# Kernel optimization log

Measured on AMD Instinct MI355X. Metric: run time of the kernel, lower is better.

The kernel has to match this reference:

```python
import jax, jax.numpy as jnp
import numpy as np

B = 16384    # batch of game states
HAND = 8     # max_hand_size
A = 30       # max_actions
C = 4        # max cards per action combo
E = 32       # card_embed_dim
HID = 128    # hidden_dim


def _encode_cards(cards, val_emb, suit_emb, type_emb):
    # cards: int array, 0 = padding, 53 = joker (treated as padding for value/suit)
    invalid = (cards == 0) | (cards == 53)
    values = jnp.where(invalid, 0, (cards - 1) % 13 + 1)
    suits = jnp.where(invalid, 0, (cards - 1) // 13 + 1)
    ce = jnp.concatenate([val_emb[values], suit_emb[suits]], axis=-1)  # [..., E]
    ct = jnp.where(values == 11, 1, jnp.where(values == 12, 2, jnp.where(values == 13, 3, 0)))
    te = type_emb[ct]  # [..., 8]
    pad = jnp.zeros(te.shape[:-1] + (E - te.shape[-1],), ce.dtype)
    return ce + jnp.concatenate([te, pad], axis=-1)


def _mha(q, kv, wq, bq, wk, bk, wv, bv, wo, bo, nh, kpm=None):
    b, sq, e = q.shape
    sk = kv.shape[1]
    hd = e // nh
    Q = (q @ wq + bq).reshape(b, sq, nh, hd)
    K = (kv @ wk + bk).reshape(b, sk, nh, hd)
    V = (kv @ wv + bv).reshape(b, sk, nh, hd)
    s = jnp.einsum('bqhd,bkhd->bhqk', Q, K) * (1.0 / np.sqrt(hd))
    if kpm is not None:  # kpm True = valid key
        s = s + jnp.where(kpm[:, None, None, :], 0.0, -1e9)
    a = jax.nn.softmax(s, axis=-1)
    o = jnp.einsum('bhqk,bkhd->bqhd', a, V).reshape(b, sq, e)
    return o @ wo + bo


def _combo_features(cards):
    # cards: [A, C] int, 0 = padding. Vectorized version of _compute_combo_features.
    mask = cards != 0
    combo_size = mask.sum(1).astype(jnp.float32)
    values = jnp.where(mask, (cards - 1) % 13 + 1, 0)
    has_valid = mask.any(1)
    fidx = jnp.argmax(mask, axis=1)
    fv = values[jnp.arange(cards.shape[0]), fidx]  # first valid value per action
    same = jnp.where(mask, values == fv[:, None], True).all(1).astype(jnp.float32)
    vf = values.astype(jnp.float32)
    attack = jnp.where(values == 1, 1.0,
             jnp.where(values == 11, 10.0,
             jnp.where(values == 12, 15.0,
             jnp.where(values == 13, 20.0, vf))))
    total = (attack * mask).sum(1)
    suits = jnp.where(mask, (cards - 1) // 13 + 1, 0)
    uniq = jnp.stack([(suits == s).any(1) for s in (1, 2, 3, 4)], 0).sum(0).astype(jnp.float32)
    ace = ((values == 1) & mask).any(1).astype(jnp.float32)
    valid = ((combo_size <= 4.0) & ((same > 0) | (ace > 0))).astype(jnp.float32)
    feats = jnp.stack([combo_size, same, total, uniq, ace, valid], axis=1)  # [A, 6]
    return jnp.where(has_valid[:, None], feats, 0.0), has_valid


def _forward(hand_cards, enemy_card, hand_size, game_state, discard_pile_cards,
             action_card_indices, num_valid_actions,
             val_emb, suit_emb, type_emb,
             ce_w1, ce_b1, ce_w2, ce_b2,
             ha_wq, ha_bq, ha_wk, ha_bk, ha_wv, ha_bv, ha_wo, ha_bo,
             he_wq, he_bq, he_wk, he_bk, he_wv, he_bv, he_wo, he_bo,
             se_w1, se_b1, se_w2, se_b2,
             atc_w1, atc_b1, atc_w2, atc_b2,
             as_w1, as_b1, as_w2, as_b2, as_w3, as_b3,
             cx_w1, cx_b1, cx_w2, cx_b2, cx_w3, cx_b3):
    relu = jax.nn.relu
    hand_emb = _encode_cards(hand_cards, val_emb, suit_emb, type_emb)            # [B, HAND, E]
    enemy_emb = _encode_cards(enemy_card[:, None], val_emb, suit_emb, type_emb)  # [B, 1, E]
    hand_mask = hand_cards != 0
    attended = _mha(hand_emb, hand_emb, ha_wq, ha_bq, ha_wk, ha_bk, ha_wv, ha_bv, ha_wo, ha_bo, 8, kpm=hand_mask)
    ctx_he = _mha(attended, enemy_emb, he_wq, he_bq, he_wk, he_bk, he_wv, he_bv, he_wo, he_bo, 4)
    lengths = jnp.maximum(hand_size.astype(jnp.float32), 1.0)[:, None]
    hand_ctx = ctx_he.sum(1) / lengths                                           # [B, E]

    # strategic features (batched per game state)
    hvals = jnp.where(hand_cards == 0, 0, (hand_cards - 1) % 13 + 1)
    hsz = hand_size.astype(jnp.float32)
    aces = (hvals == 1).sum(1).astype(jnp.float32)
    faces = ((hvals >= 11) & (hvals <= 13)).sum(1).astype(jnp.float32)
    low = ((hvals >= 2) & (hvals <= 6)).sum(1).astype(jnp.float32)
    hsuits = jnp.where(hand_cards == 0, 0, (hand_cards - 1) // 13 + 1)
    scnt = [(hsuits == s).sum(1).astype(jnp.float32) for s in (1, 2, 3, 4)]
    hvr = faces / (hsz + 1e-8)
    sdiv = jnp.stack([(hsuits == s).any(1) for s in (1, 2, 3, 4)], 0).sum(0).astype(jnp.float32) / 4.0
    strat = jnp.stack([hsz, aces, faces, low, scnt[0], scnt[1], scnt[2], scnt[3], hvr, sdiv], axis=1)
    strat_in = jnp.concatenate([game_state, strat], axis=1)                      # [B, 20]
    strat_ctx = relu(strat_in @ se_w1 + se_b1) @ se_w2 + se_b2                   # [B, 32]

    combined = jnp.concatenate([hand_ctx, enemy_emb[:, 0], strat_ctx, discard_pile_cards], axis=1)  # [B, 150]
    h = relu(combined @ cx_w1 + cx_b1)
    h = relu(h @ cx_w2 + cx_b2)
    ctx = h @ cx_w3 + cx_b3                                                      # [B, HID]
    type_probs = jax.nn.softmax(relu(ctx @ atc_w1 + atc_b1) @ atc_w2 + atc_b2, axis=-1)  # [B, 4]

    feats, has_valid = _combo_features(action_card_indices)                      # [A, 6], [A]
    emb = _encode_cards(action_card_indices, val_emb, suit_emb, type_emb)        # [A, C, E]
    m = (action_card_indices != 0).astype(emb.dtype)[..., None]
    cnt = jnp.maximum(m.sum(1), 1.0)
    act_emb = (emb * m).sum(1) / cnt                                             # masked mean over real cards
    act_emb = jnp.where(has_valid[:, None], act_emb, 0.0)
    combo_enc = relu(feats @ ce_w1 + ce_b1) @ ce_w2 + ce_b2                      # [A, 16]

    Bn = ctx.shape[0]
    af = jnp.concatenate([
        jnp.broadcast_to(ctx[:, None, :], (Bn, A, HID)),
        jnp.broadcast_to(act_emb[None], (Bn, A, E)),
        jnp.broadcast_to(combo_enc[None], (Bn, A, 16)),
    ], axis=-1)                                                                  # [B, A, 176]
    s = relu(af @ as_w1 + as_b1)
    s = relu(s @ as_w2 + as_b2)
    score = (s @ as_w3 + as_b3)[..., 0]                                          # [B, A]

    strength = feats[:, 2] / 20.0                                                # [A]
    bonus_valid = type_probs[:, 0:1] * strength[None, :] + type_probs[:, 1:2] * (1.0 - strength[None, :])
    bonus_empty = jnp.broadcast_to(type_probs[:, 3:4] * 2.0, (Bn, A))
    bonus = jnp.where(has_valid[None, :], bonus_valid, bonus_empty)
    return score + bonus                                                          # [B, A]


def setup_inputs() -> dict:
    key = jax.random.key(0)
    ki = iter(jax.random.split(key, 64))
    def nrm(shape, s):
        return (s * jax.random.normal(next(ki), shape)).astype(jnp.float32)
    def lin(i, o, s=0.08):
        return nrm((i, o), s), nrm((o,), 0.02)
    d = {}
    hc = jax.random.randint(next(ki), (B, HAND), 0, 53)
    d['hand_cards'] = hc.at[:, 0].set(jax.random.randint(next(ki), (B,), 1, 53))  # at least one valid card per hand
    d['enemy_card'] = jax.random.randint(next(ki), (B,), 1, 53)
    d['hand_size'] = jax.random.randint(next(ki), (B,), 1, 9)
    d['game_state'] = nrm((B, 10), 1.0)
    d['discard_pile_cards'] = jax.random.uniform(next(ki), (B, 54), dtype=jnp.float32)
    d['action_card_indices'] = jax.random.randint(next(ki), (A, C), 1, 53)
    d['num_valid_actions'] = A
    d['val_emb'] = nrm((14, 16), 0.1).at[0].set(0.0)   # padding_idx=0
    d['suit_emb'] = nrm((5, 16), 0.1).at[0].set(0.0)   # padding_idx=0
    d['type_emb'] = nrm((4, 8), 0.1)
    d['ce_w1'], d['ce_b1'] = lin(6, 32)
    d['ce_w2'], d['ce_b2'] = lin(32, 16)
    for p in ('ha', 'he'):
        for t in ('q', 'k', 'v', 'o'):
            d[p + '_w' + t], d[p + '_b' + t] = lin(E, E)
    d['se_w1'], d['se_b1'] = lin(20, 64)
    d['se_w2'], d['se_b2'] = lin(64, 32)
    d['atc_w1'], d['atc_b1'] = lin(HID, 64)
    d['atc_w2'], d['atc_b2'] = lin(64, 4)
    d['as_w1'], d['as_b1'] = lin(HID + E + 16, 64)
    d['as_w2'], d['as_b2'] = lin(64, 32)
    d['as_w3'], d['as_b3'] = lin(32, 1)
    d['cx_w1'], d['cx_b1'] = lin(2 * E + 32 + 54, HID)
    d['cx_w2'], d['cx_b2'] = lin(HID, HID)
    d['cx_w3'], d['cx_b3'] = lin(HID, HID)
    return d


def reference(hand_cards, enemy_card, hand_size, game_state, discard_pile_cards,
              action_card_indices, num_valid_actions,
              val_emb, suit_emb, type_emb,
              ce_w1, ce_b1, ce_w2, ce_b2,
              ha_wq, ha_bq, ha_wk, ha_bk, ha_wv, ha_bv, ha_wo, ha_bo,
              he_wq, he_bq, he_wk, he_bk, he_wv, he_bv, he_wo, he_bo,
              se_w1, se_b1, se_w2, se_b2,
              atc_w1, atc_b1, atc_w2, atc_b2,
              as_w1, as_b1, as_w2, as_b2, as_w3, as_b3,
              cx_w1, cx_b1, cx_w2, cx_b2, cx_w3, cx_b3):
    return _forward(hand_cards, enemy_card, hand_size, game_state, discard_pile_cards,
                    action_card_indices, num_valid_actions,
                    val_emb, suit_emb, type_emb,
                    ce_w1, ce_b1, ce_w2, ce_b2,
                    ha_wq, ha_bq, ha_wk, ha_bk, ha_wv, ha_bv, ha_wo, ha_bo,
                    he_wq, he_bq, he_wk, he_bk, he_wv, he_bv, he_wo, he_bo,
                    se_w1, se_b1, se_w2, se_b2,
                    atc_w1, atc_b1, atc_w2, atc_b2,
                    as_w1, as_b1, as_w2, as_b2, as_w3, as_b3,
                    cx_w1, cx_b1, cx_w2, cx_b2, cx_w3, cx_b3)
```

## Files before the change

### kernel.cpp

```cpp
#include <hip/hip_runtime.h>
#include <math.h>


__device__ __forceinline__ void encode_card32(int c,
                                              const float* __restrict__ val_emb,
                                              const float* __restrict__ suit_emb,
                                              const float* __restrict__ type_emb,
                                              float* e) {
  bool inv = (c == 0) || (c == 53);
  int v = inv ? 0 : ((c - 1) % 13 + 1);
  int s = inv ? 0 : ((c - 1) / 13 + 1);
  int ct = (v == 11) ? 1 : (v == 12) ? 2 : (v == 13) ? 3 : 0;
#pragma unroll
  for (int i = 0; i < 16; ++i) e[i] = val_emb[v * 16 + i];
#pragma unroll
  for (int i = 0; i < 16; ++i) e[16 + i] = suit_emb[s * 16 + i];
#pragma unroll
  for (int i = 0; i < 8; ++i) e[i] += type_emb[ct * 8 + i];
}

__global__ __launch_bounds__(64) void action_kernel(
    const int* __restrict__ acards,
    const float* __restrict__ val_emb, const float* __restrict__ suit_emb,
    const float* __restrict__ type_emb,
    const float* __restrict__ ce_w1, const float* __restrict__ ce_b1,
    const float* __restrict__ ce_w2, const float* __restrict__ ce_b2,
    const float* __restrict__ as_w1, const float* __restrict__ as_b1,
    float* __restrict__ ws) {
  __shared__ float sAct[30][32];
  __shared__ float sCombo[30][16];
  const int tid = threadIdx.x;

  if (tid < 30) {
    int c[4];
#pragma unroll
    for (int i = 0; i < 4; ++i) c[i] = acards[tid * 4 + i];
    bool mask[4]; int vals[4], suits[4]; int csize = 0; bool hasv = false;
#pragma unroll
    for (int i = 0; i < 4; ++i) {
      mask[i] = (c[i] != 0);
      if (mask[i]) { csize++; hasv = true; }
      vals[i] = mask[i] ? ((c[i] - 1) % 13 + 1) : 0;
      suits[i] = mask[i] ? ((c[i] - 1) / 13 + 1) : 0;
    }
    int fvv = mask[0] ? vals[0] : mask[1] ? vals[1] : mask[2] ? vals[2]
              : mask[3] ? vals[3] : vals[0];
    bool same = true;
#pragma unroll
    for (int i = 0; i < 4; ++i) if (mask[i] && vals[i] != fvv) same = false;
    float total = 0.f;
#pragma unroll
    for (int i = 0; i < 4; ++i) {
      if (mask[i]) {
        int v = vals[i];
        total += (v == 1) ? 1.f : (v == 11) ? 10.f : (v == 12) ? 15.f
                 : (v == 13) ? 20.f : (float)v;
      }
    }
    float uniq = 0.f;
#pragma unroll
    for (int s = 1; s <= 4; ++s) {
      bool any = false;
#pragma unroll
      for (int i = 0; i < 4; ++i) if (suits[i] == s) any = true;
      uniq += any ? 1.f : 0.f;
    }
    bool ace = false;
#pragma unroll
    for (int i = 0; i < 4; ++i) if (mask[i] && vals[i] == 1) ace = true;
    float f_same = same ? 1.f : 0.f, f_ace = ace ? 1.f : 0.f;
    float valid = (((float)csize <= 4.f) && (f_same > 0.f || f_ace > 0.f)) ? 1.f : 0.f;
    float feats[6] = {(float)csize, f_same, total, uniq, f_ace, valid};
    if (!hasv) { for (int i = 0; i < 6; ++i) feats[i] = 0.f; }
    float emb[32];
#pragma unroll
    for (int i = 0; i < 32; ++i) emb[i] = 0.f;
    float cnt = 0.f;
#pragma unroll
    for (int i = 0; i < 4; ++i) {
      float e[32];
      encode_card32(c[i], val_emb, suit_emb, type_emb, e);
      if (mask[i]) {
#pragma unroll
        for (int j = 0; j < 32; ++j) emb[j] += e[j];
        cnt += 1.f;
      }
    }
    float invc = 1.f / fmaxf(cnt, 1.f);
#pragma unroll
    for (int j = 0; j < 32; ++j) sAct[tid][j] = hasv ? emb[j] * invc : 0.f;
    float t32[32];
#pragma unroll
    for (int j = 0; j < 32; ++j) {
      float acc = ce_b1[j];
#pragma unroll
      for (int k = 0; k < 6; ++k) acc += feats[k] * ce_w1[k * 32 + j];
      t32[j] = fmaxf(acc, 0.f);
    }
#pragma unroll
    for (int j = 0; j < 16; ++j) {
      float acc = ce_b2[j];
#pragma unroll
      for (int k = 0; k < 32; ++k) acc += t32[k] * ce_w2[k * 16 + j];
      sCombo[tid][j] = acc;
    }
    ws[1920 + tid] = total * 0.05f;
    ws[1950 + tid] = hasv ? 1.f : 0.f;
  }
  __syncthreads();
  for (int idx = tid; idx < 1920; idx += 64) {
    int a = idx >> 6, j = idx & 63;
    float acc = as_b1[j];
#pragma unroll
    for (int k = 0; k < 32; ++k) acc += sAct[a][k] * as_w1[(128 + k) * 64 + j];
#pragma unroll
    for (int k = 0; k < 16; ++k) acc += sCombo[a][k] * as_w1[(160 + k) * 64 + j];
    ws[idx] = acc;
  }
}

template <int K, int NJ, bool RELU, bool HASB, bool QIN, bool QOUT>
__device__ __forceinline__ void layerU(
    const float* __restrict__ in, int inColBase, float* __restrict__ outB,
    int outColBase, const float* __restrict__ W, int ldw, int j0,
    const float* __restrict__ bias, int r) {
  float acc[NJ];
#pragma unroll
  for (int j = 0; j < NJ; ++j) acc[j] = HASB ? bias[j0 + j] : 0.f;
  if constexpr (QIN) {
    static_assert(K % 4 == 0, "quad input needs K%4==0");
    const int g0 = inColBase >> 2;
#pragma unroll 4
    for (int g = 0; g < K / 4; ++g) {
      float4 a = *(const float4*)&in[(g0 + g) * 256 + r * 4];
#pragma unroll
      for (int q = 0; q < 4; ++q) {
        float av = (q == 0) ? a.x : (q == 1) ? a.y : (q == 2) ? a.z : a.w;
        const float* wr = W + (size_t)(g * 4 + q) * ldw + j0;
#pragma unroll
        for (int j = 0; j < NJ; ++j) acc[j] += av * wr[j];
      }
    }
  } else {
#pragma unroll 4
    for (int k = 0; k < K; ++k) {
      float a = in[(inColBase + k) * 64 + r];
      const float* wr = W + (size_t)k * ldw + j0;
#pragma unroll
      for (int j = 0; j < NJ; ++j) acc[j] += a * wr[j];
    }
  }
#pragma unroll
  for (int j = 0; j < NJ; ++j) if (RELU) acc[j] = fmaxf(acc[j], 0.f);
  if constexpr (QOUT && (NJ % 4 == 0)) {
    const int c0 = outColBase + j0;
#pragma unroll
    for (int qg = 0; qg < NJ / 4; ++qg) {
      float4 o = make_float4(acc[qg * 4], acc[qg * 4 + 1],
                             acc[qg * 4 + 2], acc[qg * 4 + 3]);
      *(float4*)&outB[((c0 >> 2) + qg) * 256 + r * 4] = o;
    }
  } else {
#pragma unroll
    for (int j = 0; j < NJ; ++j) outB[(outColBase + j0 + j) * 64 + r] = acc[j];
  }
}

__global__ __launch_bounds__(1024) void policy_main(
    const int* __restrict__ hand_cards, const int* __restrict__ enemy_card,
    const int* __restrict__ hand_size, const float* __restrict__ game_state,
    const float* __restrict__ discard,
    const float* __restrict__ val_emb, const float* __restrict__ suit_emb,
    const float* __restrict__ type_emb,
    const float* __restrict__ he_wv, const float* __restrict__ he_bv,
    const float* __restrict__ he_wo, const float* __restrict__ he_bo,
    const float* __restrict__ se_w1, const float* __restrict__ se_b1,
    const float* __restrict__ se_w2, const float* __restrict__ se_b2,
    const float* __restrict__ atc_w1, const float* __restrict__ atc_b1,
    const float* __restrict__ atc_w2, const float* __restrict__ atc_b2,
    const float* __restrict__ as_w1,
    const float* __restrict__ as_w2, const float* __restrict__ as_b2,
    const float* __restrict__ as_w3, const float* __restrict__ as_b3,
    const float* __restrict__ cx_w1, const float* __restrict__ cx_b1,
    const float* __restrict__ cx_w2, const float* __restrict__ cx_b2,
    const float* __restrict__ cx_w3, const float* __restrict__ cx_b3,
    const float* __restrict__ ws, float* __restrict__ out) {
  __shared__ float bufA[38 * 256];
  __shared__ float bufB[128 * 64];

  const int tid = threadIdx.x;
  const int r = tid & 63;
  const int wq = __builtin_amdgcn_readfirstlane(tid >> 6);
  const int b0 = blockIdx.x * 64;

  for (int idx = tid; idx < 64 * 54; idx += 1024) {
    int rr = idx / 54, k = idx - rr * 54;
    int c = 96 + k;
    bufA[(c >> 2) * 256 + rr * 4 + (c & 3)] = discard[(size_t)b0 * 54 + idx];
  }
  if (wq == 2) {
#pragma unroll
    for (int k = 0; k < 10; ++k)
      bufB[k * 64 + r] = game_state[(size_t)(b0 + r) * 10 + k];
  }
  if (wq == 0) {
    const int b = b0 + r;
    const float hsz = (float)hand_size[b];
    int aces = 0, faces = 0, low = 0, c1 = 0, c2 = 0, c3 = 0, c4 = 0;
#pragma unroll
    for (int i = 0; i < 8; ++i) {
      int c = hand_cards[b * 8 + i];
      int v = (c == 0) ? 0 : ((c - 1) % 13 + 1);
      int s = (c == 0) ? 0 : ((c - 1) / 13 + 1);
      aces += (v == 1);
      faces += (v >= 11 && v <= 13);
      low += (v >= 2 && v <= 6);
      c1 += (s == 1); c2 += (s == 2); c3 += (s == 3); c4 += (s == 4);
    }
    float sdiv = (float)((c1 > 0) + (c2 > 0) + (c3 > 0) + (c4 > 0)) * 0.25f;
    float hvr = (float)faces / (hsz + 1e-8f);
    bufB[(10 + 0) * 64 + r] = hsz;          bufB[(10 + 1) * 64 + r] = (float)aces;
    bufB[(10 + 2) * 64 + r] = (float)faces; bufB[(10 + 3) * 64 + r] = (float)low;
    bufB[(10 + 4) * 64 + r] = (float)c1;    bufB[(10 + 5) * 64 + r] = (float)c2;
    bufB[(10 + 6) * 64 + r] = (float)c3;    bufB[(10 + 7) * 64 + r] = (float)c4;
    bufB[(10 + 8) * 64 + r] = hvr;          bufB[(10 + 9) * 64 + r] = sdiv;
  }
  if (wq == 1) {
    const int b = b0 + r;
    bufB[116 * 64 + r] = 8.0f / fmaxf((float)hand_size[b], 1.0f);
    float e[32];
    encode_card32(enemy_card[b], val_emb, suit_emb, type_emb, e);
#pragma unroll
    for (int g = 0; g < 8; ++g) {
      float4 ev = make_float4(e[g * 4], e[g * 4 + 1], e[g * 4 + 2], e[g * 4 + 3]);
      *(float4*)&bufA[(8 + g) * 256 + r * 4] = ev;
    }
  }
  __syncthreads();

  if (wq < 8) {
    layerU<20, 8, true, true, false, false>(bufB, 0, bufB, 20, se_w1, 64,
                                            wq * 8, se_b1, r);
  } else {
    layerU<32, 4, false, true, true, false>(bufA, 32, bufB, 84, he_wv, 32,
                                            (wq - 8) * 4, he_bv, r);
  }
  __syncthreads();

  if (wq < 8) {
    layerU<64, 4, false, true, false, true>(bufB, 20, bufA, 64, se_w2, 32,
                                            wq * 4, se_b2, r);
  } else {
    const int j0 = (wq - 8) * 4;
    float acc[4];
#pragma unroll
    for (int j = 0; j < 4; ++j) acc[j] = he_bo[j0 + j];
#pragma unroll 4
    for (int k = 0; k < 32; ++k) {
      float a = bufB[(84 + k) * 64 + r];
      const float* wr = he_wo + (size_t)k * 32 + j0;
#pragma unroll
      for (int j = 0; j < 4; ++j) acc[j] += a * wr[j];
    }
    float scale = bufB[116 * 64 + r];
    float4 o = make_float4(scale * acc[0], scale * acc[1],
                           scale * acc[2], scale * acc[3]);
    *(float4*)&bufA[(j0 >> 2) * 256 + r * 4] = o;
  }
  __syncthreads();

  {
    const int j0 = wq * 8;
    float acc[8];
#pragma unroll
    for (int j = 0; j < 8; ++j) acc[j] = cx_b1[j0 + j];
#pragma unroll 4
    for (int g = 0; g < 37; ++g) {
      float4 a = *(const float4*)&bufA[g * 256 + r * 4];
#pragma unroll
      for (int q = 0; q < 4; ++q) {
        float av = (q == 0) ? a.x : (q == 1) ? a.y : (q == 2) ? a.z : a.w;
        const float* wr = cx_w1 + (size_t)(g * 4 + q) * 128 + j0;
#pragma unroll
        for (int j = 0; j < 8; ++j) acc[j] += av * wr[j];
      }
    }
    {
      float4 a = *(const float4*)&bufA[37 * 256 + r * 4];
      const float* wr0 = cx_w1 + (size_t)148 * 128 + j0;
      const float* wr1 = cx_w1 + (size_t)149 * 128 + j0;
#pragma unroll
      for (int j = 0; j < 8; ++j) acc[j] += a.x * wr0[j] + a.y * wr1[j];
    }
#pragma unroll
    for (int qg = 0; qg < 2; ++qg) {
      float4 o = make_float4(fmaxf(acc[qg * 4], 0.f), fmaxf(acc[qg * 4 + 1], 0.f),
                             fmaxf(acc[qg * 4 + 2], 0.f), fmaxf(acc[qg * 4 + 3], 0.f));
      *(float4*)&bufB[((j0 >> 2) + qg) * 256 + r * 4] = o;
    }
  }
  __syncthreads();

  layerU<128, 8, true, true, true, true>(bufB, 0, bufA, 0, cx_w2, 128, wq * 8,
                                         cx_b2, r);
  __syncthreads();

  layerU<128, 8, false, true, true, true>(bufA, 0, bufB, 0, cx_w3, 128, wq * 8,
                                          cx_b3, r);
  __syncthreads();

  if (wq < 8) {
    layerU<128, 8, true, true, true, true>(bufB, 0, bufA, 0, atc_w1, 64,
                                           wq * 8, atc_b1, r);
  } else {
    layerU<128, 8, false, false, true, true>(bufB, 0, bufA, 64, as_w1, 64,
                                             (wq - 8) * 8, nullptr, r);
  }
  __syncthreads();

  if (wq < 4) {
    float acc = atc_b2[wq];
#pragma unroll 4
    for (int g = 0; g < 16; ++g) {
      float4 t = *(const float4*)&bufA[g * 256 + r * 4];
      acc += t.x * atc_w2[(g * 4 + 0) * 4 + wq];
      acc += t.y * atc_w2[(g * 4 + 1) * 4 + wq];
      acc += t.z * atc_w2[(g * 4 + 2) * 4 + wq];
      acc += t.w * atc_w2[(g * 4 + 3) * 4 + wq];
    }
    bufB[wq * 64 + r] = acc;
  }
  __syncthreads();

  if (wq < 15) {
    float l0 = bufB[0 * 64 + r], l1 = bufB[1 * 64 + r];
    float l2 = bufB[2 * 64 + r], l3 = bufB[3 * 64 + r];
    float m = fmaxf(fmaxf(l0, l1), fmaxf(l2, l3));
    float e0 = expf(l0 - m), e1 = expf(l1 - m), e2 = expf(l2 - m), e3 = expf(l3 - m);
    float inv = 1.f / (e0 + e1 + e2 + e3);
    float tp0 = e0 * inv, tp1 = e1 * inv, tp3 = e3 * inv;

    const float b3v = as_b3[0];
#pragma unroll 1
    for (int i = 0; i < 2; ++i) {
      const int a = wq * 2 + i;
      const float* qa = ws + a * 64;
      float acc[32];
#pragma unroll
      for (int j = 0; j < 32; ++j) acc[j] = 0.f;
#pragma unroll 2
      for (int g = 0; g < 16; ++g) {
        float4 pv = *(const float4*)&bufA[(16 + g) * 256 + r * 4];
#pragma unroll
        for (int q = 0; q < 4; ++q) {
          float p = (q == 0) ? pv.x : (q == 1) ? pv.y : (q == 2) ? pv.z : pv.w;
          const int k = g * 4 + q;
          float s = fmaxf(p + qa[k], 0.f);
          const float* w2r = as_w2 + (size_t)k * 32;
#pragma unroll
          for (int j = 0; j < 32; ++j) acc[j] += s * w2r[j];
        }
      }
      float sc = b3v;
#pragma unroll
      for (int j = 0; j < 32; ++j)
        sc += fmaxf(acc[j] + as_b2[j], 0.f) * as_w3[j];
      float st = ws[1920 + a], hv = ws[1950 + a];
      float bon = (hv > 0.5f) ? (tp0 * st + tp1 * (1.f - st)) : tp3 * 2.f;
      out[(size_t)(b0 + r) * 30 + a] = sc + bon;
    }
  }
}

extern "C" void kernel_launch(void* const* d_in, const int* in_sizes, int n_in,
                              void* d_out, int out_size, void* d_ws, size_t ws_size,
                              hipStream_t stream) {
  (void)in_sizes; (void)n_in; (void)out_size; (void)ws_size;
  const int* hand_cards = (const int*)d_in[0];
  const int* enemy_card = (const int*)d_in[1];
  const int* hand_size = (const int*)d_in[2];
  const float* game_state = (const float*)d_in[3];
  const float* discard = (const float*)d_in[4];
  const int* acards = (const int*)d_in[5];
  const float* val_emb = (const float*)d_in[7];
  const float* suit_emb = (const float*)d_in[8];
  const float* type_emb = (const float*)d_in[9];
  const float* ce_w1 = (const float*)d_in[10], * ce_b1 = (const float*)d_in[11];
  const float* ce_w2 = (const float*)d_in[12], * ce_b2 = (const float*)d_in[13];
  const float* he_wv = (const float*)d_in[26], * he_bv = (const float*)d_in[27];
  const float* he_wo = (const float*)d_in[28], * he_bo = (const float*)d_in[29];
  const float* se_w1 = (const float*)d_in[30], * se_b1 = (const float*)d_in[31];
  const float* se_w2 = (const float*)d_in[32], * se_b2 = (const float*)d_in[33];
  const float* atc_w1 = (const float*)d_in[34], * atc_b1 = (const float*)d_in[35];
  const float* atc_w2 = (const float*)d_in[36], * atc_b2 = (const float*)d_in[37];
  const float* as_w1 = (const float*)d_in[38], * as_b1 = (const float*)d_in[39];
  const float* as_w2 = (const float*)d_in[40], * as_b2 = (const float*)d_in[41];
  const float* as_w3 = (const float*)d_in[42], * as_b3 = (const float*)d_in[43];
  const float* cx_w1 = (const float*)d_in[44], * cx_b1 = (const float*)d_in[45];
  const float* cx_w2 = (const float*)d_in[46], * cx_b2 = (const float*)d_in[47];
  const float* cx_w3 = (const float*)d_in[48], * cx_b3 = (const float*)d_in[49];
  float* ws = (float*)d_ws;
  float* out = (float*)d_out;

  hipLaunchKernelGGL(action_kernel, dim3(1), dim3(64), 0, stream,
                     acards, val_emb, suit_emb, type_emb,
                     ce_w1, ce_b1, ce_w2, ce_b2, as_w1, as_b1, ws);
  hipLaunchKernelGGL(policy_main, dim3(256), dim3(1024), 0, stream,
                     hand_cards, enemy_card, hand_size, game_state, discard,
                     val_emb, suit_emb, type_emb,
                     he_wv, he_bv, he_wo, he_bo,
                     se_w1, se_b1, se_w2, se_b2,
                     atc_w1, atc_b1, atc_w2, atc_b2,
                     as_w1, as_w2, as_b2, as_w3, as_b3,
                     cx_w1, cx_b1, cx_w2, cx_b2, cx_w3, cx_b3,
                     ws, out);
}
```

Baseline: 246.0 us.

## Fuse batch-independent action encoding into main kernel, drop separate launch

Removes the single-block action_kernel and recomputes the action-combo encoding and the as_w1 action projection inside every policy_main block, keeping the results in shared memory instead of the global workspace. The he_wv layer is remapped onto 4 waves with 8 columns each, which frees 4 waves to compute the action projection. The final scoring loop now handles two actions per pass and shares each as_w2 weight load between them. This removes one kernel launch and its serial dependency. In exchange, every block repeats the small action computation and uses more shared memory.

```diff
diff --git a/kernel.cpp b/kernel.cpp
--- a/kernel.cpp
+++ b/kernel.cpp
@@ -19,106 +19,6 @@
   for (int i = 0; i < 8; ++i) e[i] += type_emb[ct * 8 + i];
 }
 
-__global__ __launch_bounds__(64) void action_kernel(
-    const int* __restrict__ acards,
-    const float* __restrict__ val_emb, const float* __restrict__ suit_emb,
-    const float* __restrict__ type_emb,
-    const float* __restrict__ ce_w1, const float* __restrict__ ce_b1,
-    const float* __restrict__ ce_w2, const float* __restrict__ ce_b2,
-    const float* __restrict__ as_w1, const float* __restrict__ as_b1,
-    float* __restrict__ ws) {
-  __shared__ float sAct[30][32];
-  __shared__ float sCombo[30][16];
-  const int tid = threadIdx.x;
-
-  if (tid < 30) {
-    int c[4];
-#pragma unroll
-    for (int i = 0; i < 4; ++i) c[i] = acards[tid * 4 + i];
-    bool mask[4]; int vals[4], suits[4]; int csize = 0; bool hasv = false;
-#pragma unroll
-    for (int i = 0; i < 4; ++i) {
-      mask[i] = (c[i] != 0);
-      if (mask[i]) { csize++; hasv = true; }
-      vals[i] = mask[i] ? ((c[i] - 1) % 13 + 1) : 0;
-      suits[i] = mask[i] ? ((c[i] - 1) / 13 + 1) : 0;
-    }
-    int fvv = mask[0] ? vals[0] : mask[1] ? vals[1] : mask[2] ? vals[2]
-              : mask[3] ? vals[3] : vals[0];
-    bool same = true;
-#pragma unroll
-    for (int i = 0; i < 4; ++i) if (mask[i] && vals[i] != fvv) same = false;
-    float total = 0.f;
-#pragma unroll
-    for (int i = 0; i < 4; ++i) {
-      if (mask[i]) {
-        int v = vals[i];
-        total += (v == 1) ? 1.f : (v == 11) ? 10.f : (v == 12) ? 15.f
-                 : (v == 13) ? 20.f : (float)v;
-      }
-    }
-    float uniq = 0.f;
-#pragma unroll
-    for (int s = 1; s <= 4; ++s) {
-      bool any = false;
-#pragma unroll
-      for (int i = 0; i < 4; ++i) if (suits[i] == s) any = true;
-      uniq += any ? 1.f : 0.f;
-    }
-    bool ace = false;
-#pragma unroll
-    for (int i = 0; i < 4; ++i) if (mask[i] && vals[i] == 1) ace = true;
-    float f_same = same ? 1.f : 0.f, f_ace = ace ? 1.f : 0.f;
-    float valid = (((float)csize <= 4.f) && (f_same > 0.f || f_ace > 0.f)) ? 1.f : 0.f;
-    float feats[6] = {(float)csize, f_same, total, uniq, f_ace, valid};
-    if (!hasv) { for (int i = 0; i < 6; ++i) feats[i] = 0.f; }
-    float emb[32];
-#pragma unroll
-    for (int i = 0; i < 32; ++i) emb[i] = 0.f;
-    float cnt = 0.f;
-#pragma unroll
-    for (int i = 0; i < 4; ++i) {
-      float e[32];
-      encode_card32(c[i], val_emb, suit_emb, type_emb, e);
-      if (mask[i]) {
-#pragma unroll
-        for (int j = 0; j < 32; ++j) emb[j] += e[j];
-        cnt += 1.f;
-      }
-    }
-    float invc = 1.f / fmaxf(cnt, 1.f);
-#pragma unroll
-    for (int j = 0; j < 32; ++j) sAct[tid][j] = hasv ? emb[j] * invc : 0.f;
-    float t32[32];
-#pragma unroll
-    for (int j = 0; j < 32; ++j) {
-      float acc = ce_b1[j];
-#pragma unroll
-      for (int k = 0; k < 6; ++k) acc += feats[k] * ce_w1[k * 32 + j];
-      t32[j] = fmaxf(acc, 0.f);
-    }
-#pragma unroll
-    for (int j = 0; j < 16; ++j) {
-      float acc = ce_b2[j];
-#pragma unroll
-      for (int k = 0; k < 32; ++k) acc += t32[k] * ce_w2[k * 16 + j];
-      sCombo[tid][j] = acc;
-    }
-    ws[1920 + tid] = total * 0.05f;
-    ws[1950 + tid] = hasv ? 1.f : 0.f;
-  }
-  __syncthreads();
-  for (int idx = tid; idx < 1920; idx += 64) {
-    int a = idx >> 6, j = idx & 63;
-    float acc = as_b1[j];
-#pragma unroll
-    for (int k = 0; k < 32; ++k) acc += sAct[a][k] * as_w1[(128 + k) * 64 + j];
-#pragma unroll
-    for (int k = 0; k < 16; ++k) acc += sCombo[a][k] * as_w1[(160 + k) * 64 + j];
-    ws[idx] = acc;
-  }
-}
-
 template <int K, int NJ, bool RELU, bool HASB, bool QIN, bool QOUT>
 __device__ __forceinline__ void layerU(
     const float* __restrict__ in, int inColBase, float* __restrict__ outB,
@@ -169,24 +69,29 @@
 __global__ __launch_bounds__(1024) void policy_main(
     const int* __restrict__ hand_cards, const int* __restrict__ enemy_card,
     const int* __restrict__ hand_size, const float* __restrict__ game_state,
-    const float* __restrict__ discard,
+    const float* __restrict__ discard, const int* __restrict__ acards,
     const float* __restrict__ val_emb, const float* __restrict__ suit_emb,
     const float* __restrict__ type_emb,
+    const float* __restrict__ ce_w1, const float* __restrict__ ce_b1,
+    const float* __restrict__ ce_w2, const float* __restrict__ ce_b2,
     const float* __restrict__ he_wv, const float* __restrict__ he_bv,
     const float* __restrict__ he_wo, const float* __restrict__ he_bo,
     const float* __restrict__ se_w1, const float* __restrict__ se_b1,
     const float* __restrict__ se_w2, const float* __restrict__ se_b2,
     const float* __restrict__ atc_w1, const float* __restrict__ atc_b1,
     const float* __restrict__ atc_w2, const float* __restrict__ atc_b2,
-    const float* __restrict__ as_w1,
+    const float* __restrict__ as_w1, const float* __restrict__ as_b1,
     const float* __restrict__ as_w2, const float* __restrict__ as_b2,
     const float* __restrict__ as_w3, const float* __restrict__ as_b3,
     const float* __restrict__ cx_w1, const float* __restrict__ cx_b1,
     const float* __restrict__ cx_w2, const float* __restrict__ cx_b2,
     const float* __restrict__ cx_w3, const float* __restrict__ cx_b3,
-    const float* __restrict__ ws, float* __restrict__ out) {
+    float* __restrict__ out) {
   __shared__ float bufA[38 * 256];
   __shared__ float bufB[128 * 64];
+  __shared__ float sScr[30 * 48];
+  __shared__ float sQa[30 * 68];
+  __shared__ float sMeta[64];
 
   const int tid = threadIdx.x;
   const int r = tid & 63;
@@ -236,14 +141,112 @@
       *(float4*)&bufA[(8 + g) * 256 + r * 4] = ev;
     }
   }
+  if (wq == 3 && r < 30) {
+    int c[4];
+#pragma unroll
+    for (int i = 0; i < 4; ++i) c[i] = acards[r * 4 + i];
+    bool mask[4]; int vals[4], suits[4]; int csize = 0; bool hasv = false;
+#pragma unroll
+    for (int i = 0; i < 4; ++i) {
+      mask[i] = (c[i] != 0);
+      if (mask[i]) { csize++; hasv = true; }
+      vals[i] = mask[i] ? ((c[i] - 1) % 13 + 1) : 0;
+      suits[i] = mask[i] ? ((c[i] - 1) / 13 + 1) : 0;
+    }
+    int fvv = mask[0] ? vals[0] : mask[1] ? vals[1] : mask[2] ? vals[2]
+              : mask[3] ? vals[3] : vals[0];
+    bool same = true;
+#pragma unroll
+    for (int i = 0; i < 4; ++i) if (mask[i] && vals[i] != fvv) same = false;
+    float total = 0.f;
+#pragma unroll
+    for (int i = 0; i < 4; ++i) {
+      if (mask[i]) {
+        int v = vals[i];
+        total += (v == 1) ? 1.f : (v == 11) ? 10.f : (v == 12) ? 15.f
+                 : (v == 13) ? 20.f : (float)v;
+      }
+    }
+    float uniq = 0.f;
+#pragma unroll
+    for (int s = 1; s <= 4; ++s) {
+      bool any = false;
+#pragma unroll
+      for (int i = 0; i < 4; ++i) if (suits[i] == s) any = true;
+      uniq += any ? 1.f : 0.f;
+    }
+    bool ace = false;
+#pragma unroll
+    for (int i = 0; i < 4; ++i) if (mask[i] && vals[i] == 1) ace = true;
+    float f_same = same ? 1.f : 0.f, f_ace = ace ? 1.f : 0.f;
+    float valid = (((float)csize <= 4.f) && (f_same > 0.f || f_ace > 0.f)) ? 1.f : 0.f;
+    float feats[6] = {(float)csize, f_same, total, uniq, f_ace, valid};
+    if (!hasv) { for (int i = 0; i < 6; ++i) feats[i] = 0.f; }
+    float emb[32];
+#pragma unroll
+    for (int i = 0; i < 32; ++i) emb[i] = 0.f;
+    float cnt = 0.f;
+#pragma unroll
+    for (int i = 0; i < 4; ++i) {
+      float e[32];
+      encode_card32(c[i], val_emb, suit_emb, type_emb, e);
+      if (mask[i]) {
+#pragma unroll
+        for (int j = 0; j < 32; ++j) emb[j] += e[j];
+        cnt += 1.f;
+      }
+    }
+    float invc = 1.f / fmaxf(cnt, 1.f);
+#pragma unroll
+    for (int j = 0; j < 32; ++j)
+      sScr[r * 48 + j] = hasv ? emb[j] * invc : 0.f;
+    float t32[32];
+#pragma unroll
+    for (int j = 0; j < 32; ++j) {
+      float acc = ce_b1[j];
+#pragma unroll
+      for (int k = 0; k < 6; ++k) acc += feats[k] * ce_w1[k * 32 + j];
+      t32[j] = fmaxf(acc, 0.f);
+    }
+#pragma unroll
+    for (int j = 0; j < 16; ++j) {
+      float acc = ce_b2[j];
+#pragma unroll
+      for (int k = 0; k < 32; ++k) acc += t32[k] * ce_w2[k * 16 + j];
+      sScr[r * 48 + 32 + j] = acc;
+    }
+    sMeta[r] = total * 0.05f;
+    sMeta[32 + r] = hasv ? 1.f : 0.f;
+  }
   __syncthreads();
 
   if (wq < 8) {
     layerU<20, 8, true, true, false, false>(bufB, 0, bufB, 20, se_w1, 64,
                                             wq * 8, se_b1, r);
-  } else {
-    layerU<32, 4, false, true, true, false>(bufA, 32, bufB, 84, he_wv, 32,
-                                            (wq - 8) * 4, he_bv, r);
+  } else if (wq < 12) {
+    layerU<32, 8, false, true, true, false>(bufA, 32, bufB, 84, he_wv, 32,
+                                            (wq - 8) * 8, he_bv, r);
+  } else if (r < 30) {
+    const int j0 = (wq - 12) * 16;
+    float acc[16];
+#pragma unroll
+    for (int j = 0; j < 16; ++j) acc[j] = as_b1[j0 + j];
+#pragma unroll 4
+    for (int k = 0; k < 32; ++k) {
+      float a = sScr[r * 48 + k];
+      const float* wr = as_w1 + (size_t)(128 + k) * 64 + j0;
+#pragma unroll
+      for (int j = 0; j < 16; ++j) acc[j] += a * wr[j];
+    }
+#pragma unroll
+    for (int k = 0; k < 16; ++k) {
+      float a = sScr[r * 48 + 32 + k];
+      const float* wr = as_w1 + (size_t)(160 + k) * 64 + j0;
+#pragma unroll
+      for (int j = 0; j < 16; ++j) acc[j] += a * wr[j];
+    }
+#pragma unroll
+    for (int j = 0; j < 16; ++j) sQa[r * 68 + j0 + j] = acc[j];
   }
   __syncthreads();
 
@@ -304,11 +307,9 @@
   layerU<128, 8, true, true, true, true>(bufB, 0, bufA, 0, cx_w2, 128, wq * 8,
                                          cx_b2, r);
   __syncthreads();
-
   layerU<128, 8, false, true, true, true>(bufA, 0, bufB, 0, cx_w3, 128, wq * 8,
                                           cx_b3, r);
   __syncthreads();
-
   if (wq < 8) {
     layerU<128, 8, true, true, true, true>(bufB, 0, bufA, 0, atc_w1, 64,
                                            wq * 8, atc_b1, r);
@@ -340,42 +341,52 @@
     float inv = 1.f / (e0 + e1 + e2 + e3);
     float tp0 = e0 * inv, tp1 = e1 * inv, tp3 = e3 * inv;
 
-    const float b3v = as_b3[0];
-#pragma unroll 1
-    for (int i = 0; i < 2; ++i) {
-      const int a = wq * 2 + i;
-      const float* qa = ws + a * 64;
-      float acc[32];
-#pragma unroll
-      for (int j = 0; j < 32; ++j) acc[j] = 0.f;
+    const int a0 = wq * 2, a1 = a0 + 1;
+    float acc0[32], acc1[32];
+#pragma unroll
+    for (int j = 0; j < 32; ++j) { acc0[j] = 0.f; acc1[j] = 0.f; }
 #pragma unroll 2
-      for (int g = 0; g < 16; ++g) {
-        float4 pv = *(const float4*)&bufA[(16 + g) * 256 + r * 4];
-#pragma unroll
-        for (int q = 0; q < 4; ++q) {
-          float p = (q == 0) ? pv.x : (q == 1) ? pv.y : (q == 2) ? pv.z : pv.w;
-          const int k = g * 4 + q;
-          float s = fmaxf(p + qa[k], 0.f);
-          const float* w2r = as_w2 + (size_t)k * 32;
-#pragma unroll
-          for (int j = 0; j < 32; ++j) acc[j] += s * w2r[j];
+    for (int g = 0; g < 16; ++g) {
+      float4 pv = *(const float4*)&bufA[(16 + g) * 256 + r * 4];
+      float4 q0 = *(const float4*)&sQa[a0 * 68 + g * 4];
+      float4 q1 = *(const float4*)&sQa[a1 * 68 + g * 4];
+#pragma unroll
+      for (int q = 0; q < 4; ++q) {
+        float p  = (q == 0) ? pv.x : (q == 1) ? pv.y : (q == 2) ? pv.z : pv.w;
+        float qa0v = (q == 0) ? q0.x : (q == 1) ? q0.y : (q == 2) ? q0.z : q0.w;
+        float qa1v = (q == 0) ? q1.x : (q == 1) ? q1.y : (q == 2) ? q1.z : q1.w;
+        float s0 = fmaxf(p + qa0v, 0.f);
+        float s1 = fmaxf(p + qa1v, 0.f);
+        const float* w2r = as_w2 + (size_t)(g * 4 + q) * 32;
+#pragma unroll
+        for (int j = 0; j < 32; ++j) {
+          float w = w2r[j];
+          acc0[j] += s0 * w;
+          acc1[j] += s1 * w;
         }
       }
-      float sc = b3v;
-#pragma unroll
-      for (int j = 0; j < 32; ++j)
-        sc += fmaxf(acc[j] + as_b2[j], 0.f) * as_w3[j];
-      float st = ws[1920 + a], hv = ws[1950 + a];
-      float bon = (hv > 0.5f) ? (tp0 * st + tp1 * (1.f - st)) : tp3 * 2.f;
-      out[(size_t)(b0 + r) * 30 + a] = sc + bon;
-    }
+    }
+    const float b3v = as_b3[0];
+    float sc0 = b3v, sc1 = b3v;
+#pragma unroll
+    for (int j = 0; j < 32; ++j) {
+      float bb2 = as_b2[j], w3 = as_w3[j];
+      sc0 += fmaxf(acc0[j] + bb2, 0.f) * w3;
+      sc1 += fmaxf(acc1[j] + bb2, 0.f) * w3;
+    }
+    float st0 = sMeta[a0], hv0 = sMeta[32 + a0];
+    float st1 = sMeta[a1], hv1 = sMeta[32 + a1];
+    float bon0 = (hv0 > 0.5f) ? (tp0 * st0 + tp1 * (1.f - st0)) : tp3 * 2.f;
+    float bon1 = (hv1 > 0.5f) ? (tp0 * st1 + tp1 * (1.f - st1)) : tp3 * 2.f;
+    out[(size_t)(b0 + r) * 30 + a0] = sc0 + bon0;
+    out[(size_t)(b0 + r) * 30 + a1] = sc1 + bon1;
   }
 }
 
 extern "C" void kernel_launch(void* const* d_in, const int* in_sizes, int n_in,
                               void* d_out, int out_size, void* d_ws, size_t ws_size,
                               hipStream_t stream) {
-  (void)in_sizes; (void)n_in; (void)out_size; (void)ws_size;
+  (void)in_sizes; (void)n_in; (void)out_size; (void)d_ws; (void)ws_size;
   const int* hand_cards = (const int*)d_in[0];
   const int* enemy_card = (const int*)d_in[1];
   const int* hand_size = (const int*)d_in[2];
@@ -399,19 +410,16 @@
   const float* cx_w1 = (const float*)d_in[44], * cx_b1 = (const float*)d_in[45];
   const float* cx_w2 = (const float*)d_in[46], * cx_b2 = (const float*)d_in[47];
   const float* cx_w3 = (const float*)d_in[48], * cx_b3 = (const float*)d_in[49];
-  float* ws = (float*)d_ws;
   float* out = (float*)d_out;
 
-  hipLaunchKernelGGL(action_kernel, dim3(1), dim3(64), 0, stream,
-                     acards, val_emb, suit_emb, type_emb,
-                     ce_w1, ce_b1, ce_w2, ce_b2, as_w1, as_b1, ws);
   hipLaunchKernelGGL(policy_main, dim3(256), dim3(1024), 0, stream,
                      hand_cards, enemy_card, hand_size, game_state, discard,
-                     val_emb, suit_emb, type_emb,
+                     acards, val_emb, suit_emb, type_emb,
+                     ce_w1, ce_b1, ce_w2, ce_b2,
                      he_wv, he_bv, he_wo, he_bo,
                      se_w1, se_b1, se_w2, se_b2,
                      atc_w1, atc_b1, atc_w2, atc_b2,
-                     as_w1, as_w2, as_b2, as_w3, as_b3,
+                     as_w1, as_b1, as_w2, as_b2, as_w3, as_b3,
                      cx_w1, cx_b1, cx_w2, cx_b2, cx_w3, cx_b3,
-                     ws, out);
+                     out);
 }
```

Measured after the change: 240.1 us. -2.4%, faster.
